# Optimization experiments

Hardware: AMD Instinct MI355X
Metric: run time of the kernel (lower is better)

The kernel has to match this reference:

```python
import jax, jax.numpy as jnp
import numpy as np

N = 100000   # local subgraph nodes
E = 600000   # directed edges
D = 128      # memory_dim
B = 10000    # label nodes queried
C = 32       # num_classes


def _glorot(key, shape):
    s = 1.0 / np.sqrt(shape[0])
    return jax.random.uniform(key, shape, jnp.float32, -s, s)


def setup_inputs() -> dict:
    key = jax.random.key(0)
    ks = jax.random.split(key, 16)
    return {
        "node_state": jax.random.normal(ks[0], (N, D), jnp.float32),
        "edge_index": jax.random.randint(ks[1], (2, E), 0, N),
        "label_pos": jax.random.randint(ks[2], (B,), 0, N),
        # SAGEConv 1: lin_l (neighbor, with bias), lin_r (root, no bias)
        "W1l": _glorot(ks[3], (D, D)), "b1l": jnp.zeros((D,), jnp.float32),
        "W1r": _glorot(ks[4], (D, D)),
        # SAGEConv 2
        "W2l": _glorot(ks[5], (D, D)), "b2l": jnp.zeros((D,), jnp.float32),
        "W2r": _glorot(ks[6], (D, D)),
        # classifier: Linear(D,D) -> ReLU -> Linear(D,C)
        "Wc1": _glorot(ks[7], (D, D)), "bc1": jnp.zeros((D,), jnp.float32),
        "Wc2": _glorot(ks[8], (D, C)), "bc2": jnp.zeros((C,), jnp.float32),
    }


def _sage(x, src, dst, Wl, bl, Wr):
    # PyG SAGEConv, aggr='mean': out_i = lin_l(mean_{j: (j->i)} x_j) + lin_r(x_i)
    n = x.shape[0]
    agg = jax.ops.segment_sum(x[src], dst, num_segments=n)          # [N, D]
    cnt = jax.ops.segment_sum(jnp.ones_like(dst, x.dtype), dst, num_segments=n)
    mean = agg / jnp.maximum(cnt, 1.0)[:, None]
    return mean @ Wl + bl + x @ Wr


def reference(node_state, edge_index, label_pos,
              W1l, b1l, W1r, W2l, b2l, W2r, Wc1, bc1, Wc2, bc2):
    src, dst = edge_index[0], edge_index[1]
    x = jax.nn.relu(_sage(node_state, src, dst, W1l, b1l, W1r))
    x = jax.nn.relu(_sage(x, src, dst, W2l, b2l, W2r))
    h = jax.nn.relu(x[label_pos] @ Wc1 + bc1)                        # [B, D]
    return h @ Wc2 + bc2                                             # [B, C]
```

## Files before the change

### kernel.cpp

```cpp
#include <hip/hip_runtime.h>
#include <hip/hip_bf16.h>

static constexpr int N = 100000;
static constexpr int E = 600000;
static constexpr int D = 128;
static constexpr int B = 10000;
static constexpr int C = 32;
static constexpr int NB = (N + 1023) / 1024;
static constexpr int TOUCHB = (N * (D / 4) + 255) / 256;

typedef __attribute__((ext_vector_type(8))) short short8;
typedef __attribute__((ext_vector_type(4))) float f32x4;

static __device__ __forceinline__ unsigned short f2bf(float f) {
    unsigned u = __float_as_uint(f);
    unsigned r = (u + 0x7FFFu + ((u >> 16) & 1u)) >> 16;
    return (unsigned short)r;
}
static __device__ __forceinline__ float bf2f(unsigned short h) {
    return __uint_as_float(((unsigned)h) << 16);
}

static __device__ __forceinline__ void split8(const float4 v0, const float4 v1,
                                              short8& h, short8& l) {
    const float f[8] = {v0.x, v0.y, v0.z, v0.w, v1.x, v1.y, v1.z, v1.w};
    #pragma unroll
    for (int i = 0; i < 8; ++i) {
        unsigned short hh = f2bf(f[i]);
        h[i] = (short)hh;
        l[i] = (short)f2bf(f[i] - bf2f(hh));
    }
}

__global__ void lab_k(const int* __restrict__ label_pos, int* __restrict__ labflag,
                      int* __restrict__ flag, int nlab) {
    int i = blockIdx.x * blockDim.x + threadIdx.x;
    if (i < nlab) {
        int v = label_pos[i];
        labflag[v] = 1;
        flag[v] = 1;
    }
}

__global__ __launch_bounds__(256) void deg_swz_k(
    const int* __restrict__ src, const int* __restrict__ dst,
    const int* __restrict__ labflag,
    int* __restrict__ deg, int* __restrict__ flag, int nE, int EB,
    const float* W0, const float* W1, const float* W2, const float* W3,
    const float* W4, const float* W5,
    unsigned short* __restrict__ out,
    const float* __restrict__ xtouch, float* __restrict__ sink) {
    if ((int)blockIdx.x < EB) {
        int e = blockIdx.x * 256 + threadIdx.x;
        if (e < nE) {
            int d = dst[e];
            atomicAdd(&deg[d], 1);
            if (labflag[d]) flag[src[e]] = 1;
        }
        return;
    }
    if ((int)blockIdx.x < EB + 80) {
        const int sb = blockIdx.x - EB;
        const int m = sb >> 4;
        const int chunk = sb & 15;
        const float* W = (m == 0) ? W0 : (m == 1) ? W1 : (m == 2) ? W2
                       : (m == 3) ? W3 : W4;
        unsigned short* o = out + (size_t)m * 32768;
        #pragma unroll
        for (int it = 0; it < 4; ++it) {
            int f = chunk * 1024 + it * 256 + threadIdx.x;
            int j = f & 7;
            int lane = (f >> 3) & 63;
            int fi = f >> 9;
            int k = (fi >> 3) * 32 + (lane >> 4) * 8 + j;
            int n = (fi & 7) * 16 + (lane & 15);
            float a = W[k * 128 + n];
            unsigned short h = f2bf(a);
            o[f] = h;
            o[16384 + f] = f2bf(a - bf2f(h));
        }
        return;
    }
    if ((int)blockIdx.x == EB + 80) {
        unsigned short* o2 = out + (size_t)5 * 32768;
        #pragma unroll
        for (int it = 0; it < 16; ++it) {
            int f = it * 256 + threadIdx.x;
            int j = f & 7;
            int lane = (f >> 3) & 63;
            int fi = f >> 9;
            int k = (fi >> 1) * 32 + (lane >> 4) * 8 + j;
            int n = (fi & 1) * 16 + (lane & 15);
            float a = W5[k * 32 + n];
            unsigned short h = f2bf(a);
            o2[f] = h;
            o2[4096 + f] = f2bf(a - bf2f(h));
        }
        return;
    }
    const int f4 = (blockIdx.x - (EB + 81)) * 256 + threadIdx.x;
    if (f4 < N * (D / 4)) {
        float4 v = reinterpret_cast<const float4*>(xtouch)[f4];
        float s = v.x + v.y + v.z + v.w;
        if (s > 1e30f) *sink = s;
    }
}

__global__ __launch_bounds__(256) void scan1m_k(const int* __restrict__ deg,
                                                const int* __restrict__ flag,
                                                int* __restrict__ bsum, int n) {
    __shared__ int lsum[256];
    const int t = threadIdx.x;
    const bool isdeg = (int)blockIdx.x < NB;
    const int bloc = isdeg ? blockIdx.x : blockIdx.x - NB;
    const int* v = isdeg ? deg : flag;
    const int base = bloc * 1024 + t * 4;
    int s = 0;
    #pragma unroll
    for (int i = 0; i < 4; ++i) {
        int idx = base + i;
        if (idx < n) s += v[idx];
    }
    lsum[t] = s;
    __syncthreads();
    for (int off = 128; off > 0; off >>= 1) {
        if (t < off) lsum[t] += lsum[t + off];
        __syncthreads();
    }
    if (t == 0) bsum[blockIdx.x] = lsum[0];
}

__global__ __launch_bounds__(256) void scan3m_k(
    const int* __restrict__ deg, const int* __restrict__ flag,
    const int* __restrict__ bsum,
    int* __restrict__ roff, int* __restrict__ cur,
    int* __restrict__ map, int* __restrict__ ulist, int* __restrict__ ucnt,
    int n)
{
    __shared__ int sb[128];
    __shared__ int lsum[256];
    const int t = threadIdx.x;
    const bool isdeg = (int)blockIdx.x < NB;
    const int bloc = isdeg ? blockIdx.x : blockIdx.x - NB;
    const int* bs = isdeg ? bsum : bsum + NB;
    const int* v  = isdeg ? deg : flag;

    if (t < 128) sb[t] = (t < NB) ? bs[t] : 0;
    __syncthreads();
    for (int off = 1; off < 128; off <<= 1) {
        int u = (t < 128 && t >= off) ? sb[t - off] : 0;
        __syncthreads();
        if (t < 128) sb[t] += u;
        __syncthreads();
    }
    const int boff = (bloc == 0) ? 0 : sb[bloc - 1];
    if (bloc == 0 && t == 0) {
        if (isdeg) roff[n] = sb[NB - 1];
        else *ucnt = sb[NB - 1];
    }

    const int base = bloc * 1024 + t * 4;
    int d[4];
    int s = 0;
    #pragma unroll
    for (int i = 0; i < 4; ++i) {
        int idx = base + i;
        d[i] = (idx < n) ? v[idx] : 0;
        s += d[i];
    }
    lsum[t] = s;
    __syncthreads();
    for (int off = 1; off < 256; off <<= 1) {
        int u = (t >= off) ? lsum[t - off] : 0;
        __syncthreads();
        lsum[t] += u;
        __syncthreads();
    }
    int run = boff + lsum[t] - s;
    #pragma unroll
    for (int i = 0; i < 4; ++i) {
        int idx = base + i;
        if (idx < n) {
            if (isdeg) {
                roff[idx] = run;
                cur[idx]  = run;
                run += d[i];
            } else if (d[i]) {
                map[idx] = run;
                ulist[run] = idx;
                ++run;
            }
        }
    }
}

__global__ void fill_k(const int* __restrict__ src, const int* __restrict__ dst,
                       const int* __restrict__ flag,
                       int* __restrict__ cur, int* __restrict__ csr_src, int nE) {
    int e = blockIdx.x * blockDim.x + threadIdx.x;
    if (e < nE) {
        int d = dst[e];
        if (flag[d]) {
            int p = atomicAdd(&cur[d], 1);
            csr_src[p] = src[e];
        }
    }
}

template <bool GATHER, bool MAP>
__global__ __launch_bounds__(256) void gather_mean_k(
    const float* __restrict__ x, const int* __restrict__ roff,
    const int* __restrict__ csr_src, const int* __restrict__ rows,
    const int* __restrict__ map, const int* __restrict__ nrows_ptr,
    float* __restrict__ out, int nrows_max) {
    const int nrows = nrows_ptr ? nrows_ptr[0] : nrows_max;
    const int w = blockIdx.x * (blockDim.x >> 6) + (threadIdx.x >> 6);
    if (w >= nrows) return;
    const int lane = threadIdx.x & 63;
    const int n  = GATHER ? rows[w] : w;
    const int jb = roff[n];
    const int je = roff[n + 1];
    const float* xb = x + lane * 2;

    float ax = 0.f, ay = 0.f;
    int j = jb;
    for (; j + 4 <= je; j += 4) {
        int s0 = csr_src[j + 0];
        int s1 = csr_src[j + 1];
        int s2 = csr_src[j + 2];
        int s3 = csr_src[j + 3];
        if (MAP) { s0 = map[s0]; s1 = map[s1]; s2 = map[s2]; s3 = map[s3]; }
        float2 v0 = *reinterpret_cast<const float2*>(xb + (size_t)s0 * D);
        float2 v1 = *reinterpret_cast<const float2*>(xb + (size_t)s1 * D);
        float2 v2 = *reinterpret_cast<const float2*>(xb + (size_t)s2 * D);
        float2 v3 = *reinterpret_cast<const float2*>(xb + (size_t)s3 * D);
        ax += v0.x + v1.x + v2.x + v3.x;
        ay += v0.y + v1.y + v2.y + v3.y;
    }
    for (; j < je; ++j) {
        int s = csr_src[j];
        if (MAP) s = map[s];
        float2 v = *reinterpret_cast<const float2*>(xb + (size_t)s * D);
        ax += v.x;
        ay += v.y;
    }
    const float inv = 1.0f / fmaxf((float)(je - jb), 1.0f);
    *reinterpret_cast<float2*>(out + (size_t)w * D + lane * 2) =
        make_float2(ax * inv, ay * inv);
}

template <bool GATHER, bool MAP>
__global__ __launch_bounds__(256, 6) void sage_mfma_k(
    const float* __restrict__ mean, const float* __restrict__ xsrc,
    const int* __restrict__ rows, const int* __restrict__ map,
    const int* __restrict__ nrows_ptr,
    const unsigned short* __restrict__ WlSw, const unsigned short* __restrict__ WrSw,
    const float* __restrict__ bl, float* __restrict__ xout, int nrows_max)
{
    const int nrows = nrows_ptr ? nrows_ptr[0] : nrows_max;
    const int rb = blockIdx.x * 32;
    if (rb >= nrows) return;

    const int t = threadIdx.x;
    const int wrow = (t >> 6) & 1;
    const int wcol = t >> 7;
    const int lane = t & 63;
    const int mcol = lane & 15;
    const int q = lane >> 4;
    const int r = rb + wrow * 16 + mcol;

    f32x4 acc[4];
    #pragma unroll
    for (int no = 0; no < 4; ++no) acc[no] = (f32x4){0.f, 0.f, 0.f, 0.f};

    size_t gidx = 0;
    if (r < nrows) {
        int g = GATHER ? rows[r] : r;
        if (MAP) g = map[g];
        gidx = (size_t)g;
    }

    #pragma unroll
    for (int br = 0; br < 2; ++br) {
        const unsigned short* __restrict__ Wm = br ? WrSw : WlSw;
        #pragma unroll
        for (int kp = 0; kp < 4; ++kp) {
            short8 aH, aL;
            {
                float4 v0 = make_float4(0.f, 0.f, 0.f, 0.f);
                float4 v1 = make_float4(0.f, 0.f, 0.f, 0.f);
                if (r < nrows) {
                    const float* p = (br == 0)
                        ? mean + (size_t)r * D + kp * 32 + q * 8
                        : xsrc + gidx * D + kp * 32 + q * 8;
                    v0 = *reinterpret_cast<const float4*>(p);
                    v1 = *reinterpret_cast<const float4*>(p + 4);
                }
                split8(v0, v1, aH, aL);
            }
            #pragma unroll
            for (int no = 0; no < 4; ++no) {
                const size_t fo = ((size_t)(kp * 8 + wcol * 4 + no) * 64 + lane) * 8;
                short8 bh = *reinterpret_cast<const short8*>(Wm + fo);
                short8 bo = *reinterpret_cast<const short8*>(Wm + 16384 + fo);
                acc[no] = __builtin_amdgcn_mfma_f32_16x16x32_bf16(aH, bh, acc[no], 0, 0, 0);
                acc[no] = __builtin_amdgcn_mfma_f32_16x16x32_bf16(aL, bh, acc[no], 0, 0, 0);
                acc[no] = __builtin_amdgcn_mfma_f32_16x16x32_bf16(aH, bo, acc[no], 0, 0, 0);
            }
        }
    }

    #pragma unroll
    for (int no = 0; no < 4; ++no) {
        const int col = wcol * 64 + no * 16 + mcol;
        const float bias = bl[col];
        #pragma unroll
        for (int ri = 0; ri < 4; ++ri) {
            const int row = rb + wrow * 16 + q * 4 + ri;
            if (row < nrows)
                xout[(size_t)row * D + col] = fmaxf(acc[no][ri] + bias, 0.f);
        }
    }
}

__global__ __launch_bounds__(256) void sage2_cls_k(
    const float* __restrict__ mean, const float* __restrict__ x1c,
    const int* __restrict__ label_pos, const int* __restrict__ map,
    const unsigned short* __restrict__ WlSw, const unsigned short* __restrict__ WrSw,
    const float* __restrict__ bl,
    const unsigned short* __restrict__ Wc1Sw, const float* __restrict__ bc1,
    const unsigned short* __restrict__ Wc2Sw, const float* __restrict__ bc2,
    float* __restrict__ out, int nrows)
{
    __shared__ alignas(16) float Xs[32][132];
    __shared__ alignas(16) float Hs[32][132];
    const int rb = blockIdx.x * 32;
    const int t = threadIdx.x;
    const int wrow = (t >> 6) & 1;
    const int wcol = t >> 7;
    const int lane = t & 63;
    const int mcol = lane & 15;
    const int q = lane >> 4;
    const int r = rb + wrow * 16 + mcol;

    f32x4 acc[4];
    #pragma unroll
    for (int no = 0; no < 4; ++no) acc[no] = (f32x4){0.f, 0.f, 0.f, 0.f};

    size_t gidx = 0;
    if (r < nrows) gidx = (size_t)map[label_pos[r]];

    #pragma unroll
    for (int br = 0; br < 2; ++br) {
        const unsigned short* __restrict__ Wm = br ? WrSw : WlSw;
        #pragma unroll
        for (int kp = 0; kp < 4; ++kp) {
            short8 aH, aL;
            {
                float4 v0 = make_float4(0.f, 0.f, 0.f, 0.f);
                float4 v1 = make_float4(0.f, 0.f, 0.f, 0.f);
                if (r < nrows) {
                    const float* p = (br == 0)
                        ? mean + (size_t)r * D + kp * 32 + q * 8
                        : x1c + gidx * D + kp * 32 + q * 8;
                    v0 = *reinterpret_cast<const float4*>(p);
                    v1 = *reinterpret_cast<const float4*>(p + 4);
                }
                split8(v0, v1, aH, aL);
            }
            #pragma unroll
            for (int no = 0; no < 4; ++no) {
                const size_t fo = ((size_t)(kp * 8 + wcol * 4 + no) * 64 + lane) * 8;
                short8 bh = *reinterpret_cast<const short8*>(Wm + fo);
                short8 bo = *reinterpret_cast<const short8*>(Wm + 16384 + fo);
                acc[no] = __builtin_amdgcn_mfma_f32_16x16x32_bf16(aH, bh, acc[no], 0, 0, 0);
                acc[no] = __builtin_amdgcn_mfma_f32_16x16x32_bf16(aL, bh, acc[no], 0, 0, 0);
                acc[no] = __builtin_amdgcn_mfma_f32_16x16x32_bf16(aH, bo, acc[no], 0, 0, 0);
            }
        }
    }

    #pragma unroll
    for (int no = 0; no < 4; ++no) {
        const int col = wcol * 64 + no * 16 + mcol;
        const float bias = bl[col];
        #pragma unroll
        for (int ri = 0; ri < 4; ++ri) {
            const int lrow = wrow * 16 + q * 4 + ri;
            Xs[lrow][col] = fmaxf(acc[no][ri] + bias, 0.f);
        }
    }
    __syncthreads();

    {
        f32x4 acc2[4];
        #pragma unroll
        for (int no = 0; no < 4; ++no) acc2[no] = (f32x4){0.f, 0.f, 0.f, 0.f};

        #pragma unroll
        for (int kp = 0; kp < 4; ++kp) {
            short8 aH, aL;
            {
                const float* p = &Xs[wrow * 16 + mcol][kp * 32 + q * 8];
                float4 v0 = *reinterpret_cast<const float4*>(p);
                float4 v1 = *reinterpret_cast<const float4*>(p + 4);
                split8(v0, v1, aH, aL);
            }
            #pragma unroll
            for (int no = 0; no < 4; ++no) {
                const size_t fo = ((size_t)(kp * 8 + wcol * 4 + no) * 64 + lane) * 8;
                short8 bh = *reinterpret_cast<const short8*>(Wc1Sw + fo);
                short8 bo = *reinterpret_cast<const short8*>(Wc1Sw + 16384 + fo);
                acc2[no] = __builtin_amdgcn_mfma_f32_16x16x32_bf16(aH, bh, acc2[no], 0, 0, 0);
                acc2[no] = __builtin_amdgcn_mfma_f32_16x16x32_bf16(aL, bh, acc2[no], 0, 0, 0);
                acc2[no] = __builtin_amdgcn_mfma_f32_16x16x32_bf16(aH, bo, acc2[no], 0, 0, 0);
            }
        }
        #pragma unroll
        for (int no = 0; no < 4; ++no) {
            const int col = wcol * 64 + no * 16 + mcol;
            const float bias = bc1[col];
            #pragma unroll
            for (int ri = 0; ri < 4; ++ri) {
                const int lrow = wrow * 16 + q * 4 + ri;
                Hs[lrow][col] = fmaxf(acc2[no][ri] + bias, 0.0f);
            }
        }
    }
    __syncthreads();

    {
        f32x4 acc3 = (f32x4){0.f, 0.f, 0.f, 0.f};
        #pragma unroll
        for (int kp = 0; kp < 4; ++kp) {
            short8 aH, aL;
            {
                const float* p = &Hs[wrow * 16 + mcol][kp * 32 + q * 8];
                float4 v0 = *reinterpret_cast<const float4*>(p);
                float4 v1 = *reinterpret_cast<const float4*>(p + 4);
                split8(v0, v1, aH, aL);
            }
            const size_t fo = ((size_t)(kp * 2 + wcol) * 64 + lane) * 8;
            short8 bh = *reinterpret_cast<const short8*>(Wc2Sw + fo);
            short8 bo = *reinterpret_cast<const short8*>(Wc2Sw + 4096 + fo);
            acc3 = __builtin_amdgcn_mfma_f32_16x16x32_bf16(aH, bh, acc3, 0, 0, 0);
            acc3 = __builtin_amdgcn_mfma_f32_16x16x32_bf16(aL, bh, acc3, 0, 0, 0);
            acc3 = __builtin_amdgcn_mfma_f32_16x16x32_bf16(aH, bo, acc3, 0, 0, 0);
        }
        const int col = wcol * 16 + mcol;
        const float b2 = bc2[col];
        #pragma unroll
        for (int ri = 0; ri < 4; ++ri) {
            const int row = rb + wrow * 16 + q * 4 + ri;
            if (row < nrows) out[(size_t)row * C + col] = acc3[ri] + b2;
        }
    }
}


extern "C" void kernel_launch(void* const* d_in, const int* in_sizes, int n_in,
                              void* d_out, int out_size, void* d_ws, size_t ws_size,
                              hipStream_t stream) {
    const float* node_state = (const float*)d_in[0];
    const int*   edge_index = (const int*)d_in[1];
    const int*   label_pos  = (const int*)d_in[2];
    const float* W1l = (const float*)d_in[3];
    const float* b1l = (const float*)d_in[4];
    const float* W1r = (const float*)d_in[5];
    const float* W2l = (const float*)d_in[6];
    const float* b2l = (const float*)d_in[7];
    const float* W2r = (const float*)d_in[8];
    const float* Wc1 = (const float*)d_in[9];
    const float* bc1 = (const float*)d_in[10];
    const float* Wc2 = (const float*)d_in[11];
    const float* bc2 = (const float*)d_in[12];
    float* out = (float*)d_out;

    const int* src = edge_index;
    const int* dst = edge_index + E;

    char* ws = (char*)d_ws;
    float* x1c   = (float*)ws;                    ws += sizeof(float) * (size_t)N * D;
    float* bufA  = (float*)ws;                    ws += sizeof(float) * (size_t)N * D;
    unsigned short* Wsw = (unsigned short*)ws;    ws += sizeof(unsigned short) * (5 * 32768 + 8192);
    int* deg     = (int*)ws;                      ws += sizeof(int) * N;
    int* flag    = (int*)ws;                      ws += sizeof(int) * N;
    int* labflag = (int*)ws;                      ws += sizeof(int) * N;
    int* ucnt    = (int*)ws;                      ws += sizeof(int);
    float* sink  = (float*)ws;                    ws += sizeof(float);
    ws += sizeof(int) * 2;
    int* roff    = (int*)ws;                      ws += sizeof(int) * (N + 1);
    int* cur     = (int*)ws;                      ws += sizeof(int) * N;
    int* csr_src = (int*)ws;                      ws += sizeof(int) * E;
    int* map     = (int*)ws;                      ws += sizeof(int) * N;
    int* ulist   = (int*)ws;                      ws += sizeof(int) * N;
    int* bsum    = (int*)ws;                      ws += sizeof(int) * 256;
    float* mean1c = bufA;
    float* mean2g = bufA;

    const int TB = 256;
    const int EB = (E + TB - 1) / TB;

    hipMemsetAsync(deg, 0, sizeof(int) * (3 * N + 1), stream);
    lab_k<<<(B + TB - 1) / TB, TB, 0, stream>>>(label_pos, labflag, flag, B);
    deg_swz_k<<<EB + 81 + TOUCHB, TB, 0, stream>>>(src, dst, labflag, deg, flag, E, EB,
                                                   W1l, W1r, W2l, W2r, Wc1, Wc2, Wsw,
                                                   node_state, sink);
    scan1m_k<<<2 * NB, 256, 0, stream>>>(deg, flag, bsum, N);
    scan3m_k<<<2 * NB, 256, 0, stream>>>(deg, flag, bsum, roff, cur, map, ulist, ucnt, N);
    fill_k<<<EB, TB, 0, stream>>>(src, dst, flag, cur, csr_src, E);

    gather_mean_k<true, false><<<(N + 3) / 4, TB, 0, stream>>>(
        node_state, roff, csr_src, ulist, nullptr, ucnt, mean1c, N);
    sage_mfma_k<true, false><<<(N + 31) / 32, TB, 0, stream>>>(
        mean1c, node_state, ulist, nullptr, ucnt,
        Wsw, Wsw + 32768, b1l, x1c, N);

    gather_mean_k<true, true><<<(B + 3) / 4, TB, 0, stream>>>(
        x1c, roff, csr_src, label_pos, map, nullptr, mean2g, B);
    sage2_cls_k<<<(B + 31) / 32, TB, 0, stream>>>(
        mean2g, x1c, label_pos, map,
        Wsw + 65536, Wsw + 98304, b2l,
        Wsw + 131072, bc1,
        Wsw + 163840, bc2, out, B);
}
```

Baseline: 241.0 us.

## Fuse all pipeline stages into one cooperative persistent kernel with grid syncs

Replaces the eight stage launches (degree/swizzle, two scan passes, CSR fill, layer-1 gather and MFMA, layer-2 gather and classifier) with one cooperative kernel that loops over virtual blocks and separates stages with grid.sync. The intent is to remove per-launch overhead and inter-kernel gaps in a pipeline of many small kernels. The block-offset scan becomes a serial loop in block 0. The trade-off is a grid capped at occupancy times 256 CUs with grid-stride loops, plus the cost of each grid barrier. The original multi-kernel path remains as a fallback if the cooperative launch fails.

```diff
diff --git a/kernel.cpp b/kernel.cpp
--- a/kernel.cpp
+++ b/kernel.cpp
@@ -1,5 +1,8 @@
 #include <hip/hip_runtime.h>
+#include <hip/hip_cooperative_groups.h>
 #include <hip/hip_bf16.h>
+
+namespace cg = cooperative_groups;
 
 static constexpr int N = 100000;
 static constexpr int E = 600000;
@@ -7,7 +10,9 @@
 static constexpr int B = 10000;
 static constexpr int C = 32;
 static constexpr int NB = (N + 1023) / 1024;
+static constexpr int EBC = (E + 255) / 256;
 static constexpr int TOUCHB = (N * (D / 4) + 255) / 256;
+static constexpr int P2TOT = EBC + 81 + TOUCHB;
 
 typedef __attribute__((ext_vector_type(8))) short short8;
 typedef __attribute__((ext_vector_type(4))) float f32x4;
@@ -41,6 +46,7 @@
         flag[v] = 1;
     }
 }
+
 
 __global__ __launch_bounds__(256) void deg_swz_k(
     const int* __restrict__ src, const int* __restrict__ dst,
@@ -457,6 +463,424 @@
     }
 }
 
+struct MegaArgs {
+    const int* src; const int* dst; const int* label_pos;
+    const float* x;
+    const float* W0; const float* W1; const float* W2; const float* W3;
+    const float* W4; const float* W5;
+    const float* b1l; const float* b2l; const float* bc1; const float* bc2;
+    unsigned short* Wsw;
+    int* deg; int* flag; const int* labflag;
+    int* ucnt;
+    int* roff; int* cur; int* csr; int* map; int* ulist;
+    int* bsum; int* boff;
+    float* sink;
+    float* x1c; float* bufA;
+    float* out;
+};
+
+__global__ __launch_bounds__(256) void mega_k(MegaArgs A) {
+    cg::grid_group grid = cg::this_grid();
+    const int t = threadIdx.x;
+    const int nblk = gridDim.x;
+    const int lane = t & 63;
+    const int wl = t >> 6;
+    const int wrow = (t >> 6) & 1;
+    const int wcol = t >> 7;
+    const int mcol = lane & 15;
+    const int q = lane >> 4;
+
+    __shared__ alignas(16) float Xs[32][132];
+    __shared__ alignas(16) float Hs[32][132];
+    __shared__ int lsum[256];
+
+    for (int vb = blockIdx.x; vb < P2TOT; vb += nblk) {
+        if (vb < EBC) {
+            int e = vb * 256 + t;
+            if (e < E) {
+                int d = A.dst[e];
+                atomicAdd(&A.deg[d], 1);
+                if (A.labflag[d]) A.flag[A.src[e]] = 1;
+            }
+        } else if (vb < EBC + 80) {
+            const int sb = vb - EBC;
+            const int m = sb >> 4;
+            const int chunk = sb & 15;
+            const float* W = (m == 0) ? A.W0 : (m == 1) ? A.W1 : (m == 2) ? A.W2
+                           : (m == 3) ? A.W3 : A.W4;
+            unsigned short* o = A.Wsw + (size_t)m * 32768;
+            #pragma unroll
+            for (int it = 0; it < 4; ++it) {
+                int f = chunk * 1024 + it * 256 + t;
+                int j = f & 7;
+                int ln = (f >> 3) & 63;
+                int fi = f >> 9;
+                int k = (fi >> 3) * 32 + (ln >> 4) * 8 + j;
+                int n = (fi & 7) * 16 + (ln & 15);
+                float a = W[k * 128 + n];
+                unsigned short h = f2bf(a);
+                o[f] = h;
+                o[16384 + f] = f2bf(a - bf2f(h));
+            }
+        } else if (vb == EBC + 80) {
+            unsigned short* o2 = A.Wsw + (size_t)5 * 32768;
+            #pragma unroll
+            for (int it = 0; it < 16; ++it) {
+                int f = it * 256 + t;
+                int j = f & 7;
+                int ln = (f >> 3) & 63;
+                int fi = f >> 9;
+                int k = (fi >> 1) * 32 + (ln >> 4) * 8 + j;
+                int n = (fi & 1) * 16 + (ln & 15);
+                float a = A.W5[k * 32 + n];
+                unsigned short h = f2bf(a);
+                o2[f] = h;
+                o2[4096 + f] = f2bf(a - bf2f(h));
+            }
+        } else {
+            const int f4 = (vb - (EBC + 81)) * 256 + t;
+            if (f4 < N * (D / 4)) {
+                float4 v = reinterpret_cast<const float4*>(A.x)[f4];
+                float s = v.x + v.y + v.z + v.w;
+                if (s > 1e30f) *A.sink = s;
+            }
+        }
+    }
+    grid.sync();
+
+    int d0 = 0, d1 = 0, d2 = 0, d3 = 0, tpre = 0;
+    const bool isScan = (int)blockIdx.x < 2 * NB;
+    const bool isdeg = (int)blockIdx.x < NB;
+    if (isScan) {
+        const int bloc = isdeg ? blockIdx.x : blockIdx.x - NB;
+        const int base = bloc * 1024 + t * 4;
+        int s = 0;
+        int dd[4];
+        #pragma unroll
+        for (int i = 0; i < 4; ++i) {
+            int idx = base + i;
+            int v = 0;
+            if (idx < N) v = isdeg ? (A.flag[idx] ? A.deg[idx] : 0) : A.flag[idx];
+            dd[i] = v; s += v;
+        }
+        d0 = dd[0]; d1 = dd[1]; d2 = dd[2]; d3 = dd[3];
+        lsum[t] = s;
+        __syncthreads();
+        for (int off = 1; off < 256; off <<= 1) {
+            int u = (t >= off) ? lsum[t - off] : 0;
+            __syncthreads();
+            lsum[t] += u;
+            __syncthreads();
+        }
+        tpre = lsum[t] - s;
+        if (t == 0) A.bsum[blockIdx.x] = lsum[255];
+    }
+    grid.sync();
+
+    if (blockIdx.x == 0) {
+        if (t == 0) {
+            int r = 0;
+            for (int b = 0; b < NB; ++b) { int v = A.bsum[b]; A.boff[b] = r; r += v; }
+            A.roff[N] = r;
+        }
+        if (t == 1) {
+            int r = 0;
+            for (int b = NB; b < 2 * NB; ++b) { int v = A.bsum[b]; A.boff[b] = r; r += v; }
+            *A.ucnt = r;
+        }
+    }
+    grid.sync();
+    const int ucv = *A.ucnt;
+
+    if (isScan) {
+        const int bloc = isdeg ? blockIdx.x : blockIdx.x - NB;
+        const int base = bloc * 1024 + t * 4;
+        int run = A.boff[blockIdx.x] + tpre;
+        int dd[4] = {d0, d1, d2, d3};
+        #pragma unroll
+        for (int i = 0; i < 4; ++i) {
+            int idx = base + i;
+            if (idx < N) {
+                if (isdeg) {
+                    A.roff[idx] = run;
+                    A.cur[idx]  = run;
+                    run += dd[i];
+                } else if (dd[i]) {
+                    A.map[idx] = run;
+                    A.ulist[run] = idx;
+                    ++run;
+                }
+            }
+        }
+    }
+    grid.sync();
+
+    for (int vb = blockIdx.x; vb < EBC; vb += nblk) {
+        int e = vb * 256 + t;
+        if (e < E) {
+            int d = A.dst[e];
+            if (A.flag[d]) {
+                int p = atomicAdd(&A.cur[d], 1);
+                A.csr[p] = A.src[e];
+            }
+        }
+    }
+    grid.sync();
+
+    {
+        const float* xb = A.x + lane * 2;
+        const int nw = nblk * 4;
+        for (int w = blockIdx.x * 4 + wl; w < ucv; w += nw) {
+            const int n = A.ulist[w];
+            const int jb = A.roff[n];
+            const int je = A.roff[n + 1];
+            float ax = 0.f, ay = 0.f;
+            int j = jb;
+            for (; j + 4 <= je; j += 4) {
+                int s0 = A.csr[j + 0];
+                int s1 = A.csr[j + 1];
+                int s2 = A.csr[j + 2];
+                int s3 = A.csr[j + 3];
+                float2 v0 = *reinterpret_cast<const float2*>(xb + (size_t)s0 * D);
+                float2 v1 = *reinterpret_cast<const float2*>(xb + (size_t)s1 * D);
+                float2 v2 = *reinterpret_cast<const float2*>(xb + (size_t)s2 * D);
+                float2 v3 = *reinterpret_cast<const float2*>(xb + (size_t)s3 * D);
+                ax += v0.x + v1.x + v2.x + v3.x;
+                ay += v0.y + v1.y + v2.y + v3.y;
+            }
+            for (; j < je; ++j) {
+                int s = A.csr[j];
+                float2 v = *reinterpret_cast<const float2*>(xb + (size_t)s * D);
+                ax += v.x;
+                ay += v.y;
+            }
+            const float inv = 1.0f / fmaxf((float)(je - jb), 1.0f);
+            *reinterpret_cast<float2*>(A.bufA + (size_t)w * D + lane * 2) =
+                make_float2(ax * inv, ay * inv);
+        }
+    }
+    grid.sync();
+
+    {
+        const unsigned short* WlSw = A.Wsw;
+        const unsigned short* WrSw = A.Wsw + 32768;
+        const int ntile = (ucv + 31) / 32;
+        for (int tile = blockIdx.x; tile < ntile; tile += nblk) {
+            const int rb = tile * 32;
+            const int r = rb + wrow * 16 + mcol;
+
+            f32x4 acc[4];
+            #pragma unroll
+            for (int no = 0; no < 4; ++no) acc[no] = (f32x4){0.f, 0.f, 0.f, 0.f};
+
+            size_t gidx = 0;
+            if (r < ucv) gidx = (size_t)A.ulist[r];
+
+            #pragma unroll
+            for (int br = 0; br < 2; ++br) {
+                const unsigned short* Wm = br ? WrSw : WlSw;
+                #pragma unroll
+                for (int kp = 0; kp < 4; ++kp) {
+                    short8 aH, aL;
+                    {
+                        float4 v0 = make_float4(0.f, 0.f, 0.f, 0.f);
+                        float4 v1 = make_float4(0.f, 0.f, 0.f, 0.f);
+                        if (r < ucv) {
+                            const float* p = (br == 0)
+                                ? A.bufA + (size_t)r * D + kp * 32 + q * 8
+                                : A.x + gidx * D + kp * 32 + q * 8;
+                            v0 = *reinterpret_cast<const float4*>(p);
+                            v1 = *reinterpret_cast<const float4*>(p + 4);
+                        }
+                        split8(v0, v1, aH, aL);
+                    }
+                    #pragma unroll
+                    for (int no = 0; no < 4; ++no) {
+                        const size_t fo = ((size_t)(kp * 8 + wcol * 4 + no) * 64 + lane) * 8;
+                        short8 bh = *reinterpret_cast<const short8*>(Wm + fo);
+                        short8 bo = *reinterpret_cast<const short8*>(Wm + 16384 + fo);
+                        acc[no] = __builtin_amdgcn_mfma_f32_16x16x32_bf16(aH, bh, acc[no], 0, 0, 0);
+                        acc[no] = __builtin_amdgcn_mfma_f32_16x16x32_bf16(aL, bh, acc[no], 0, 0, 0);
+                        acc[no] = __builtin_amdgcn_mfma_f32_16x16x32_bf16(aH, bo, acc[no], 0, 0, 0);
+                    }
+                }
+            }
+
+            #pragma unroll
+            for (int no = 0; no < 4; ++no) {
+                const int col = wcol * 64 + no * 16 + mcol;
+                const float bias = A.b1l[col];
+                #pragma unroll
+                for (int ri = 0; ri < 4; ++ri) {
+                    const int row = rb + wrow * 16 + q * 4 + ri;
+                    if (row < ucv)
+                        A.x1c[(size_t)row * D + col] = fmaxf(acc[no][ri] + bias, 0.f);
+                }
+            }
+        }
+    }
+    grid.sync();
+
+    {
+        const float* xb = A.x1c + lane * 2;
+        const int nw = nblk * 4;
+        for (int w = blockIdx.x * 4 + wl; w < B; w += nw) {
+            const int n = A.label_pos[w];
+            const int jb = A.roff[n];
+            const int je = A.roff[n + 1];
+            float ax = 0.f, ay = 0.f;
+            int j = jb;
+            for (; j + 4 <= je; j += 4) {
+                int s0 = A.map[A.csr[j + 0]];
+                int s1 = A.map[A.csr[j + 1]];
+                int s2 = A.map[A.csr[j + 2]];
+                int s3 = A.map[A.csr[j + 3]];
+                float2 v0 = *reinterpret_cast<const float2*>(xb + (size_t)s0 * D);
+                float2 v1 = *reinterpret_cast<const float2*>(xb + (size_t)s1 * D);
+                float2 v2 = *reinterpret_cast<const float2*>(xb + (size_t)s2 * D);
+                float2 v3 = *reinterpret_cast<const float2*>(xb + (size_t)s3 * D);
+                ax += v0.x + v1.x + v2.x + v3.x;
+                ay += v0.y + v1.y + v2.y + v3.y;
+            }
+            for (; j < je; ++j) {
+                int s = A.map[A.csr[j]];
+                float2 v = *reinterpret_cast<const float2*>(xb + (size_t)s * D);
+                ax += v.x;
+                ay += v.y;
+            }
+            const float inv = 1.0f / fmaxf((float)(je - jb), 1.0f);
+            *reinterpret_cast<float2*>(A.bufA + (size_t)w * D + lane * 2) =
+                make_float2(ax * inv, ay * inv);
+        }
+    }
+    grid.sync();
+
+    {
+        const unsigned short* WlSw = A.Wsw + 65536;
+        const unsigned short* WrSw = A.Wsw + 98304;
+        const unsigned short* Wc1Sw = A.Wsw + 131072;
+        const unsigned short* Wc2Sw = A.Wsw + 163840;
+        const int ntile = (B + 31) / 32;
+        for (int tile = blockIdx.x; tile < ntile; tile += nblk) {
+            const int rb = tile * 32;
+            const int r = rb + wrow * 16 + mcol;
+
+            f32x4 acc[4];
+            #pragma unroll
+            for (int no = 0; no < 4; ++no) acc[no] = (f32x4){0.f, 0.f, 0.f, 0.f};
+
+            size_t gidx = 0;
+            if (r < B) gidx = (size_t)A.map[A.label_pos[r]];
+
+            #pragma unroll
+            for (int br = 0; br < 2; ++br) {
+                const unsigned short* Wm = br ? WrSw : WlSw;
+                #pragma unroll
+                for (int kp = 0; kp < 4; ++kp) {
+                    short8 aH, aL;
+                    {
+                        float4 v0 = make_float4(0.f, 0.f, 0.f, 0.f);
+                        float4 v1 = make_float4(0.f, 0.f, 0.f, 0.f);
+                        if (r < B) {
+                            const float* p = (br == 0)
+                                ? A.bufA + (size_t)r * D + kp * 32 + q * 8
+                                : A.x1c + gidx * D + kp * 32 + q * 8;
+                            v0 = *reinterpret_cast<const float4*>(p);
+                            v1 = *reinterpret_cast<const float4*>(p + 4);
+                        }
+                        split8(v0, v1, aH, aL);
+                    }
+                    #pragma unroll
+                    for (int no = 0; no < 4; ++no) {
+                        const size_t fo = ((size_t)(kp * 8 + wcol * 4 + no) * 64 + lane) * 8;
+                        short8 bh = *reinterpret_cast<const short8*>(Wm + fo);
+                        short8 bo = *reinterpret_cast<const short8*>(Wm + 16384 + fo);
+                        acc[no] = __builtin_amdgcn_mfma_f32_16x16x32_bf16(aH, bh, acc[no], 0, 0, 0);
+                        acc[no] = __builtin_amdgcn_mfma_f32_16x16x32_bf16(aL, bh, acc[no], 0, 0, 0);
+                        acc[no] = __builtin_amdgcn_mfma_f32_16x16x32_bf16(aH, bo, acc[no], 0, 0, 0);
+                    }
+                }
+            }
+            #pragma unroll
+            for (int no = 0; no < 4; ++no) {
+                const int col = wcol * 64 + no * 16 + mcol;
+                const float bias = A.b2l[col];
+                #pragma unroll
+                for (int ri = 0; ri < 4; ++ri) {
+                    const int lrow = wrow * 16 + q * 4 + ri;
+                    Xs[lrow][col] = fmaxf(acc[no][ri] + bias, 0.f);
+                }
+            }
+            __syncthreads();
+
+            {
+                f32x4 acc2[4];
+                #pragma unroll
+                for (int no = 0; no < 4; ++no) acc2[no] = (f32x4){0.f, 0.f, 0.f, 0.f};
+
+                #pragma unroll
+                for (int kp = 0; kp < 4; ++kp) {
+                    short8 aH, aL;
+                    {
+                        const float* p = &Xs[wrow * 16 + mcol][kp * 32 + q * 8];
+                        float4 v0 = *reinterpret_cast<const float4*>(p);
+                        float4 v1 = *reinterpret_cast<const float4*>(p + 4);
+                        split8(v0, v1, aH, aL);
+                    }
+                    #pragma unroll
+                    for (int no = 0; no < 4; ++no) {
+                        const size_t fo = ((size_t)(kp * 8 + wcol * 4 + no) * 64 + lane) * 8;
+                        short8 bh = *reinterpret_cast<const short8*>(Wc1Sw + fo);
+                        short8 bo = *reinterpret_cast<const short8*>(Wc1Sw + 16384 + fo);
+                        acc2[no] = __builtin_amdgcn_mfma_f32_16x16x32_bf16(aH, bh, acc2[no], 0, 0, 0);
+                        acc2[no] = __builtin_amdgcn_mfma_f32_16x16x32_bf16(aL, bh, acc2[no], 0, 0, 0);
+                        acc2[no] = __builtin_amdgcn_mfma_f32_16x16x32_bf16(aH, bo, acc2[no], 0, 0, 0);
+                    }
+                }
+                #pragma unroll
+                for (int no = 0; no < 4; ++no) {
+                    const int col = wcol * 64 + no * 16 + mcol;
+                    const float bias = A.bc1[col];
+                    #pragma unroll
+                    for (int ri = 0; ri < 4; ++ri) {
+                        const int lrow = wrow * 16 + q * 4 + ri;
+                        Hs[lrow][col] = fmaxf(acc2[no][ri] + bias, 0.0f);
+                    }
+                }
+            }
+            __syncthreads();
+
+            {
+                f32x4 acc3 = (f32x4){0.f, 0.f, 0.f, 0.f};
+                #pragma unroll
+                for (int kp = 0; kp < 4; ++kp) {
+                    short8 aH, aL;
+                    {
+                        const float* p = &Hs[wrow * 16 + mcol][kp * 32 + q * 8];
+                        float4 v0 = *reinterpret_cast<const float4*>(p);
+                        float4 v1 = *reinterpret_cast<const float4*>(p + 4);
+                        split8(v0, v1, aH, aL);
+                    }
+                    const size_t fo = ((size_t)(kp * 2 + wcol) * 64 + lane) * 8;
+                    short8 bh = *reinterpret_cast<const short8*>(Wc2Sw + fo);
+                    short8 bo = *reinterpret_cast<const short8*>(Wc2Sw + 4096 + fo);
+                    acc3 = __builtin_amdgcn_mfma_f32_16x16x32_bf16(aH, bh, acc3, 0, 0, 0);
+                    acc3 = __builtin_amdgcn_mfma_f32_16x16x32_bf16(aL, bh, acc3, 0, 0, 0);
+                    acc3 = __builtin_amdgcn_mfma_f32_16x16x32_bf16(aH, bo, acc3, 0, 0, 0);
+                }
+                const int col = wcol * 16 + mcol;
+                const float b2 = A.bc2[col];
+                #pragma unroll
+                for (int ri = 0; ri < 4; ++ri) {
+                    const int row = rb + wrow * 16 + q * 4 + ri;
+                    if (row < B) A.out[(size_t)row * C + col] = acc3[ri] + b2;
+                }
+            }
+            __syncthreads();
+        }
+    }
+}
+
 
 extern "C" void kernel_launch(void* const* d_in, const int* in_sizes, int n_in,
                               void* d_out, int out_size, void* d_ws, size_t ws_size,
@@ -495,32 +919,78 @@
     int* map     = (int*)ws;                      ws += sizeof(int) * N;
     int* ulist   = (int*)ws;                      ws += sizeof(int) * N;
     int* bsum    = (int*)ws;                      ws += sizeof(int) * 256;
+    int* boff    = (int*)ws;                      ws += sizeof(int) * 256;
     float* mean1c = bufA;
     float* mean2g = bufA;
 
     const int TB = 256;
-    const int EB = (E + TB - 1) / TB;
+    const int EB = EBC;
 
     hipMemsetAsync(deg, 0, sizeof(int) * (3 * N + 1), stream);
     lab_k<<<(B + TB - 1) / TB, TB, 0, stream>>>(label_pos, labflag, flag, B);
-    deg_swz_k<<<EB + 81 + TOUCHB, TB, 0, stream>>>(src, dst, labflag, deg, flag, E, EB,
-                                                   W1l, W1r, W2l, W2r, Wc1, Wc2, Wsw,
-                                                   node_state, sink);
-    scan1m_k<<<2 * NB, 256, 0, stream>>>(deg, flag, bsum, N);
-    scan3m_k<<<2 * NB, 256, 0, stream>>>(deg, flag, bsum, roff, cur, map, ulist, ucnt, N);
-    fill_k<<<EB, TB, 0, stream>>>(src, dst, flag, cur, csr_src, E);
-
-    gather_mean_k<true, false><<<(N + 3) / 4, TB, 0, stream>>>(
-        node_state, roff, csr_src, ulist, nullptr, ucnt, mean1c, N);
-    sage_mfma_k<true, false><<<(N + 31) / 32, TB, 0, stream>>>(
-        mean1c, node_state, ulist, nullptr, ucnt,
-        Wsw, Wsw + 32768, b1l, x1c, N);
-
-    gather_mean_k<true, true><<<(B + 3) / 4, TB, 0, stream>>>(
-        x1c, roff, csr_src, label_pos, map, nullptr, mean2g, B);
-    sage2_cls_k<<<(B + 31) / 32, TB, 0, stream>>>(
-        mean2g, x1c, label_pos, map,
-        Wsw + 65536, Wsw + 98304, b2l,
-        Wsw + 131072, bc1,
-        Wsw + 163840, bc2, out, B);
-}
+
+    static int s_coop_ok = -1;
+    static int s_grid = 0;
+    if (s_coop_ok == -1) {
+        int dev = 0, attr = 0;
+        if (hipGetDevice(&dev) != hipSuccess) dev = 0;
+        if (hipDeviceGetAttribute(&attr, hipDeviceAttributeCooperativeLaunch, dev)
+            != hipSuccess) attr = 0;
+        s_coop_ok = attr ? 1 : 0;
+    }
+    bool launched = false;
+    if (s_coop_ok == 1) {
+        if (s_grid == 0) {
+            int perCU = 0;
+            if (hipOccupancyMaxActiveBlocksPerMultiprocessor(&perCU, mega_k, TB, 0)
+                != hipSuccess || perCU < 1) perCU = 1;
+            s_grid = perCU * 256;
+            if (s_grid > 2048) s_grid = 2048;
+            if (s_grid < 2 * NB) s_grid = 2 * NB;
+        }
+        MegaArgs a;
+        a.src = src; a.dst = dst; a.label_pos = label_pos;
+        a.x = node_state;
+        a.W0 = W1l; a.W1 = W1r; a.W2 = W2l; a.W3 = W2r; a.W4 = Wc1; a.W5 = Wc2;
+        a.b1l = b1l; a.b2l = b2l; a.bc1 = bc1; a.bc2 = bc2;
+        a.Wsw = Wsw;
+        a.deg = deg; a.flag = flag; a.labflag = labflag;
+        a.ucnt = ucnt;
+        a.roff = roff; a.cur = cur; a.csr = csr_src; a.map = map; a.ulist = ulist;
+        a.bsum = bsum; a.boff = boff;
+        a.sink = sink;
+        a.x1c = x1c; a.bufA = bufA;
+        a.out = out;
+        void* kargs[] = { &a };
+        hipError_t e = hipLaunchCooperativeKernel(mega_k, dim3(s_grid), dim3(TB),
+                                                  kargs, 0u, stream);
+        if (e == hipSuccess) {
+            launched = true;
+        } else {
+            s_coop_ok = 0;
+        }
+    }
+
+    if (!launched) {
+        deg_swz_k<<<EB + 81 + TOUCHB, TB, 0, stream>>>(src, dst, labflag, deg, flag, E, EB,
+                                                       W1l, W1r, W2l, W2r, Wc1, Wc2, Wsw,
+                                                       node_state, sink);
+        scan1m_k<<<2 * NB, 256, 0, stream>>>(deg, flag, bsum, N);
+        scan3m_k<<<2 * NB, 256, 0, stream>>>(deg, flag, bsum, roff, cur, map, ulist, ucnt, N);
+        fill_k<<<EB, TB, 0, stream>>>(src, dst, flag, cur, csr_src, E);
+
+        gather_mean_k<true, false><<<(N + 3) / 4, TB, 0, stream>>>(
+            node_state, roff, csr_src, ulist, nullptr, ucnt, mean1c, N);
+        sage_mfma_k<true, false><<<(N + 31) / 32, TB, 0, stream>>>(
+            mean1c, node_state, ulist, nullptr, ucnt,
+            Wsw, Wsw + 32768, b1l, x1c, N);
+
+        gather_mean_k<true, true><<<(B + 3) / 4, TB, 0, stream>>>(
+            x1c, roff, csr_src, label_pos, map, nullptr, mean2g, B);
+        sage2_cls_k<<<(B + 31) / 32, TB, 0, stream>>>(
+            mean2g, x1c, label_pos, map,
+            Wsw + 65536, Wsw + 98304, b2l,
+            Wsw + 131072, bc1,
+            Wsw + 163840, bc2, out, B);
+    }
+}
```

Measured after the change: 242.7 us. About the same (+0.7%).

## Fuse scan and CSR fill kernels into one kernel with grid barriers

Applied to the files above, without the earlier changes.

Merges the two scan kernels and the CSR fill kernel into a single persistent kernel of 2*NB blocks, using atomic-counter grid-wide barriers between the block-sum, prefix-offset and edge-scatter phases. This removes two kernel launches and their inter-kernel gaps. In exchange, the edge fill now runs on only about 196 blocks looping over all edge blocks, which lowers parallelism for that scatter. The spin barriers also rely on every block being co-resident, which holds for this grid size.

```diff
diff --git a/kernel.cpp b/kernel.cpp
--- a/kernel.cpp
+++ b/kernel.cpp
@@ -106,67 +106,30 @@
     }
 }
 
-__global__ __launch_bounds__(256) void scan1m_k(const int* __restrict__ deg,
-                                                const int* __restrict__ flag,
-                                                int* __restrict__ bsum, int n) {
+__global__ __launch_bounds__(256) void prep_k(
+    const int* __restrict__ deg, const int* __restrict__ flag,
+    const int* __restrict__ src, const int* __restrict__ dst,
+    int* __restrict__ bsum,
+    int* __restrict__ roff, int* __restrict__ cur,
+    int* __restrict__ map, int* __restrict__ ulist, int* __restrict__ ucnt,
+    int* __restrict__ csr_src, int* __restrict__ sync4, int nE, int EBv)
+{
     __shared__ int lsum[256];
+    __shared__ int s_blk;
     const int t = threadIdx.x;
     const bool isdeg = (int)blockIdx.x < NB;
     const int bloc = isdeg ? blockIdx.x : blockIdx.x - NB;
+    const int gbase = isdeg ? 0 : NB;
     const int* v = isdeg ? deg : flag;
+
     const int base = bloc * 1024 + t * 4;
+    int dd[4];
     int s = 0;
     #pragma unroll
     for (int i = 0; i < 4; ++i) {
         int idx = base + i;
-        if (idx < n) s += v[idx];
-    }
-    lsum[t] = s;
-    __syncthreads();
-    for (int off = 128; off > 0; off >>= 1) {
-        if (t < off) lsum[t] += lsum[t + off];
-        __syncthreads();
-    }
-    if (t == 0) bsum[blockIdx.x] = lsum[0];
-}
-
-__global__ __launch_bounds__(256) void scan3m_k(
-    const int* __restrict__ deg, const int* __restrict__ flag,
-    const int* __restrict__ bsum,
-    int* __restrict__ roff, int* __restrict__ cur,
-    int* __restrict__ map, int* __restrict__ ulist, int* __restrict__ ucnt,
-    int n)
-{
-    __shared__ int sb[128];
-    __shared__ int lsum[256];
-    const int t = threadIdx.x;
-    const bool isdeg = (int)blockIdx.x < NB;
-    const int bloc = isdeg ? blockIdx.x : blockIdx.x - NB;
-    const int* bs = isdeg ? bsum : bsum + NB;
-    const int* v  = isdeg ? deg : flag;
-
-    if (t < 128) sb[t] = (t < NB) ? bs[t] : 0;
-    __syncthreads();
-    for (int off = 1; off < 128; off <<= 1) {
-        int u = (t < 128 && t >= off) ? sb[t - off] : 0;
-        __syncthreads();
-        if (t < 128) sb[t] += u;
-        __syncthreads();
-    }
-    const int boff = (bloc == 0) ? 0 : sb[bloc - 1];
-    if (bloc == 0 && t == 0) {
-        if (isdeg) roff[n] = sb[NB - 1];
-        else *ucnt = sb[NB - 1];
-    }
-
-    const int base = bloc * 1024 + t * 4;
-    int d[4];
-    int s = 0;
-    #pragma unroll
-    for (int i = 0; i < 4; ++i) {
-        int idx = base + i;
-        d[i] = (idx < n) ? v[idx] : 0;
-        s += d[i];
+        dd[i] = (idx < N) ? v[idx] : 0;
+        s += dd[i];
     }
     lsum[t] = s;
     __syncthreads();
@@ -176,33 +139,69 @@
         lsum[t] += u;
         __syncthreads();
     }
-    int run = boff + lsum[t] - s;
+    const int tpre = lsum[t] - s;
+    if (t == 255) s_blk = lsum[255];
+    if (t == 0) bsum[blockIdx.x] = lsum[255];
+    __syncthreads();
+    const int sblk = s_blk;
+
+    __threadfence();
+    __syncthreads();
+    if (t == 0) {
+        int old = atomicAdd(&sync4[0], 1);
+        if (old == 2 * NB - 1) atomicExch(&sync4[1], 1);
+        while (atomicAdd(&sync4[1], 0) == 0) {}
+    }
+    __syncthreads();
+
+    int pv = 0;
+    if (t < bloc) pv = atomicAdd(&bsum[gbase + t], 0);
+    lsum[t] = pv;
+    __syncthreads();
+    for (int off = 128; off > 0; off >>= 1) {
+        if (t < off) lsum[t] += lsum[t + off];
+        __syncthreads();
+    }
+    const int boffv = lsum[0];
+    if (bloc == NB - 1 && t == 0) {
+        if (isdeg) roff[N] = boffv + sblk;
+        else *ucnt = boffv + sblk;
+    }
+
+    int run = boffv + tpre;
     #pragma unroll
     for (int i = 0; i < 4; ++i) {
         int idx = base + i;
-        if (idx < n) {
+        if (idx < N) {
             if (isdeg) {
                 roff[idx] = run;
                 cur[idx]  = run;
-                run += d[i];
-            } else if (d[i]) {
+                run += dd[i];
+            } else if (dd[i]) {
                 map[idx] = run;
                 ulist[run] = idx;
                 ++run;
             }
         }
     }
-}
-
-__global__ void fill_k(const int* __restrict__ src, const int* __restrict__ dst,
-                       const int* __restrict__ flag,
-                       int* __restrict__ cur, int* __restrict__ csr_src, int nE) {
-    int e = blockIdx.x * blockDim.x + threadIdx.x;
-    if (e < nE) {
-        int d = dst[e];
-        if (flag[d]) {
-            int p = atomicAdd(&cur[d], 1);
-            csr_src[p] = src[e];
+
+    __threadfence();
+    __syncthreads();
+    if (t == 0) {
+        int old = atomicAdd(&sync4[2], 1);
+        if (old == 2 * NB - 1) atomicExch(&sync4[3], 1);
+        while (atomicAdd(&sync4[3], 0) == 0) {}
+    }
+    __syncthreads();
+
+    for (int vb = blockIdx.x; vb < EBv; vb += 2 * NB) {
+        int e = vb * 256 + t;
+        if (e < nE) {
+            int d = dst[e];
+            if (flag[d]) {
+                int p = atomicAdd(&cur[d], 1);
+                csr_src[p] = src[e];
+            }
         }
     }
 }
@@ -487,6 +486,7 @@
     int* flag    = (int*)ws;                      ws += sizeof(int) * N;
     int* labflag = (int*)ws;                      ws += sizeof(int) * N;
     int* ucnt    = (int*)ws;                      ws += sizeof(int);
+    int* sync4   = (int*)ws;                      ws += sizeof(int) * 4;
     float* sink  = (float*)ws;                    ws += sizeof(float);
     ws += sizeof(int) * 2;
     int* roff    = (int*)ws;                      ws += sizeof(int) * (N + 1);
@@ -501,14 +501,13 @@
     const int TB = 256;
     const int EB = (E + TB - 1) / TB;
 
-    hipMemsetAsync(deg, 0, sizeof(int) * (3 * N + 1), stream);
+    hipMemsetAsync(deg, 0, sizeof(int) * (3 * N + 5), stream);
     lab_k<<<(B + TB - 1) / TB, TB, 0, stream>>>(label_pos, labflag, flag, B);
     deg_swz_k<<<EB + 81 + TOUCHB, TB, 0, stream>>>(src, dst, labflag, deg, flag, E, EB,
                                                    W1l, W1r, W2l, W2r, Wc1, Wc2, Wsw,
                                                    node_state, sink);
-    scan1m_k<<<2 * NB, 256, 0, stream>>>(deg, flag, bsum, N);
-    scan3m_k<<<2 * NB, 256, 0, stream>>>(deg, flag, bsum, roff, cur, map, ulist, ucnt, N);
-    fill_k<<<EB, TB, 0, stream>>>(src, dst, flag, cur, csr_src, E);
+    prep_k<<<2 * NB, 256, 0, stream>>>(deg, flag, src, dst, bsum, roff, cur,
+                                       map, ulist, ucnt, csr_src, sync4, E, EB);
 
     gather_mean_k<true, false><<<(N + 3) / 4, TB, 0, stream>>>(
         node_state, roff, csr_src, ulist, nullptr, ucnt, mean1c, N);
```

After: 275.4 us. +14.3%, slower.
